# Kernel tuning notes

Hardware: AMD Instinct MI355X
Metric: run time of the kernel (lower is better)

Reference implementation:

```python
import jax, jax.numpy as jnp
import numpy as np

N_NODES = 100000
N_EDGES = 20000
NNZ = 800000
D_IN = 256
D_OUT = 256


def _segment_mean(feats, seg_ids, num_segments):
    # feats: [nnz, d] gathered features; seg_ids: [nnz] target segment per entry
    s = jax.ops.segment_sum(feats, seg_ids, num_segments=num_segments)
    cnt = jax.ops.segment_sum(jnp.ones((seg_ids.shape[0],), feats.dtype), seg_ids,
                              num_segments=num_segments)
    return s / jnp.maximum(cnt, 1.0)[:, None]


def setup_inputs() -> dict:
    key = jax.random.key(0)
    k1, k2, k3, k4, k5 = jax.random.split(key, 5)
    X = jax.random.normal(k1, (N_NODES, D_IN), dtype=jnp.float32)
    W = jax.random.normal(k2, (D_IN, D_OUT), dtype=jnp.float32) * (1.0 / np.sqrt(D_IN))
    b = jax.random.normal(k3, (D_OUT,), dtype=jnp.float32) * 0.01
    vertex_idx = jax.random.randint(k4, (NNZ,), 0, N_NODES, dtype=jnp.int32)
    edge_idx = jax.random.randint(k5, (NNZ,), 0, N_EDGES, dtype=jnp.int32)
    return {"X": X, "W": W, "b": b, "vertex_idx": vertex_idx, "edge_idx": edge_idx}


def reference(X, W, b, vertex_idx, edge_idx):
    # theta: linear projection
    H = X @ W + b                                   # [N_NODES, D_OUT]
    # v2e mean: hyperedge feature = mean of incident vertex features
    Y = _segment_mean(H[vertex_idx], edge_idx, N_EDGES)   # [N_EDGES, D_OUT]
    # e2v mean: vertex feature = mean of incident hyperedge features
    X_ = _segment_mean(Y[edge_idx], vertex_idx, N_NODES)  # [N_NODES, D_OUT]
    # ReLU; dropout is identity in eval mode
    return jax.nn.relu(X_)
```

## Files before the change

### kernel.cpp

```cpp
#include <hip/hip_runtime.h>
#include <hip/hip_bf16.h>

constexpr int N_NODES = 100000;
constexpr int N_EDGES = 20000;
constexpr int NNZ     = 800000;
constexpr int D       = 256;

typedef unsigned short ushort_t;
typedef unsigned short ushort4v __attribute__((ext_vector_type(4)));
typedef unsigned short ushort8v __attribute__((ext_vector_type(8)));
typedef __bf16         bf16x8   __attribute__((ext_vector_type(8)));
typedef float          f32x4    __attribute__((ext_vector_type(4)));
typedef float          f32x8    __attribute__((ext_vector_type(8)));

static __device__ inline ushort_t f2bf(float f) {
  unsigned u = __builtin_bit_cast(unsigned, f);
  return (ushort_t)((u + 0x7FFFu + ((u >> 16) & 1u)) >> 16);
}

static __device__ inline f32x8 row_f32(const ushort_t* p) {
  bf16x8 b = __builtin_bit_cast(bf16x8, *(const ushort8v*)p);
  return __builtin_convertvector(b, f32x8);
}

constexpr int HIST_BLOCKS  = 782;
constexpr int TRANS_BLOCKS = 64;
constexpr int CAST_BLOCKS  = 6250;
constexpr int PREP_BLOCKS  = HIST_BLOCKS + TRANS_BLOCKS + CAST_BLOCKS;

__global__ __launch_bounds__(256) void prep_kernel(
    const float* __restrict__ X, const float* __restrict__ W,
    const int* __restrict__ vidx, const int* __restrict__ eidx,
    ushort_t* __restrict__ Xb, ushort_t* __restrict__ Wt,
    int* __restrict__ ncnt, int* __restrict__ ecnt,
    int* __restrict__ erank, int* __restrict__ nrank) {
  const int blk = blockIdx.x, tid = threadIdx.x;
  if (blk < HIST_BLOCKS) {
    int i4 = blk * 256 + tid;
    if (i4 < NNZ / 4) {
      int4 e4 = ((const int4*)eidx)[i4];
      int4 v4 = ((const int4*)vidx)[i4];
      int4 er, nr;
      er.x = atomicAdd(&ecnt[e4.x], 1);  nr.x = atomicAdd(&ncnt[v4.x], 1);
      er.y = atomicAdd(&ecnt[e4.y], 1);  nr.y = atomicAdd(&ncnt[v4.y], 1);
      er.z = atomicAdd(&ecnt[e4.z], 1);  nr.z = atomicAdd(&ncnt[v4.z], 1);
      er.w = atomicAdd(&ecnt[e4.w], 1);  nr.w = atomicAdd(&ncnt[v4.w], 1);
      ((int4*)erank)[i4] = er;
      ((int4*)nrank)[i4] = nr;
    }
  } else if (blk < HIST_BLOCKS + TRANS_BLOCKS) {
    int wb = blk - HIST_BLOCKS;
#pragma unroll
    for (int i = 0; i < 4; ++i) {
      int k = wb * 4 + i;
      Wt[(size_t)tid * 256 + k] = f2bf(W[(size_t)k * 256 + tid]);
    }
  } else {
    int cb = blk - HIST_BLOCKS - TRANS_BLOCKS;
#pragma unroll
    for (int q = 0; q < 4; ++q) {
      int idx4 = cb * 1024 + q * 256 + tid;
      float4 v = ((const float4*)X)[idx4];
      ushort4v o = { f2bf(v.x), f2bf(v.y), f2bf(v.z), f2bf(v.w) };
      *(ushort4v*)&Xb[(size_t)idx4 * 4] = o;
    }
  }
}

constexpr int SCAN_L    = N_EDGES + N_NODES;
constexpr int SCAN_TPB  = 1024;
constexpr int SCAN_EPT  = 4;
constexpr int SCAN_TILE = SCAN_TPB * SCAN_EPT;
constexpr int SCAN_NB   = (SCAN_L + SCAN_TILE - 1) / SCAN_TILE;

__global__ __launch_bounds__(1024) void scan_phaseA(
    const int* __restrict__ cnt, int* __restrict__ comb, int* __restrict__ btot) {
  __shared__ int wsum[16];
  const int tid = threadIdx.x, lane = tid & 63, wid = tid >> 6;
  const int base = blockIdx.x * SCAN_TILE + tid * SCAN_EPT;
  int v[SCAN_EPT];
#pragma unroll
  for (int i = 0; i < SCAN_EPT; ++i) {
    int j = base + i;
    v[i] = (j < SCAN_L) ? cnt[j] : 0;
  }
  int tsum = v[0] + v[1] + v[2] + v[3];
  int x = tsum;
#pragma unroll
  for (int d = 1; d < 64; d <<= 1) {
    int y = __shfl_up(x, (unsigned)d, 64);
    if (lane >= d) x += y;
  }
  if (lane == 63) wsum[wid] = x;
  __syncthreads();
  if (wid == 0) {
    int s = (lane < 16) ? wsum[lane] : 0;
#pragma unroll
    for (int d = 1; d < 16; d <<= 1) {
      int y = __shfl_up(s, (unsigned)d, 64);
      if (lane >= d) s += y;
    }
    if (lane < 16) wsum[lane] = s;
  }
  __syncthreads();
  int texcl = ((wid == 0) ? 0 : wsum[wid - 1]) + (x - tsum);
  int run = texcl;
#pragma unroll
  for (int i = 0; i < SCAN_EPT; ++i) {
    int j = base + i;
    if (j < SCAN_L) comb[j] = run;
    run += v[i];
  }
  if (tid == 0) btot[blockIdx.x] = wsum[15];
}

__global__ void scan_phaseB(const int* __restrict__ btot, int* __restrict__ boff) {
  int lane = threadIdx.x;
  int v = (lane < SCAN_NB) ? btot[lane] : 0;
  int x = v;
#pragma unroll
  for (int d = 1; d < 64; d <<= 1) {
    int y = __shfl_up(x, (unsigned)d, 64);
    if (lane >= d) x += y;
  }
  if (lane < SCAN_NB) boff[lane] = x - v;
}

__global__ __launch_bounds__(1024) void scan_phaseC(
    const int* __restrict__ comb, const int* __restrict__ boff,
    int* __restrict__ eoff, int* __restrict__ noff) {
  const int base = blockIdx.x * SCAN_TILE + threadIdx.x * SCAN_EPT;
  const int add = boff[blockIdx.x];
#pragma unroll
  for (int i = 0; i < SCAN_EPT; ++i) {
    int j = base + i;
    if (j < SCAN_L) {
      int val = comb[j] + add;
      if (j < N_EDGES) eoff[j] = val;
      else             noff[j - N_EDGES] = val - NNZ;
    }
  }
  if (blockIdx.x == 0 && threadIdx.x == 0) {
    eoff[N_EDGES] = NNZ;
    noff[N_NODES] = NNZ;
  }
}

__global__ __launch_bounds__(256) void scatter_norank(
    const int* __restrict__ vidx, const int* __restrict__ eidx,
    const int* __restrict__ eoff, const int* __restrict__ noff,
    const int* __restrict__ erank, const int* __restrict__ nrank,
    int* __restrict__ evals, int* __restrict__ nvals) {
  int i4 = blockIdx.x * 256 + threadIdx.x;
  if (i4 < NNZ / 4) {
    int4 e4 = ((const int4*)eidx)[i4];
    int4 v4 = ((const int4*)vidx)[i4];
    int4 er = ((const int4*)erank)[i4];
    int4 nr = ((const int4*)nrank)[i4];
    evals[eoff[e4.x] + er.x] = v4.x;  nvals[noff[v4.x] + nr.x] = e4.x;
    evals[eoff[e4.y] + er.y] = v4.y;  nvals[noff[v4.y] + nr.y] = e4.y;
    evals[eoff[e4.z] + er.z] = v4.z;  nvals[noff[v4.z] + nr.z] = e4.z;
    evals[eoff[e4.w] + er.w] = v4.w;  nvals[noff[v4.w] + nr.w] = e4.w;
  }
}

__global__ __launch_bounds__(256) void v2e_mean(
    const ushort_t* __restrict__ Xb, const int* __restrict__ eoff,
    const int* __restrict__ evals, ushort_t* __restrict__ Xeb, int nseg) {
  int lane = threadIdx.x & 63;
  int half = lane >> 5, l32 = lane & 31;
  int seg  = blockIdx.x * 4 + (threadIdx.x >> 6);
  if (seg >= nseg) return;
  int s = eoff[seg], e = eoff[seg + 1];
  f32x8 acc = {0, 0, 0, 0, 0, 0, 0, 0};
  int j = s + half;
  for (; j + 6 < e; j += 8) {
    int r0 = evals[j], r1 = evals[j + 2], r2 = evals[j + 4], r3 = evals[j + 6];
    f32x8 f0 = row_f32(&Xb[(size_t)r0 * 256 + l32 * 8]);
    f32x8 f1 = row_f32(&Xb[(size_t)r1 * 256 + l32 * 8]);
    f32x8 f2 = row_f32(&Xb[(size_t)r2 * 256 + l32 * 8]);
    f32x8 f3 = row_f32(&Xb[(size_t)r3 * 256 + l32 * 8]);
    acc += (f0 + f1) + (f2 + f3);
  }
  for (; j < e; j += 2)
    acc += row_f32(&Xb[(size_t)evals[j] * 256 + l32 * 8]);
  float r[8];
#pragma unroll
  for (int i = 0; i < 8; ++i) r[i] = acc[i] + __shfl_down(acc[i], 32);
  if (half == 0) {
    float inv = 1.0f / (float)max(e - s, 1);
    ushort8v o;
#pragma unroll
    for (int i = 0; i < 8; ++i) o[i] = f2bf(r[i] * inv);
    *(ushort8v*)&Xeb[(size_t)seg * 256 + l32 * 8] = o;
  }
}

__global__ __launch_bounds__(256) void gemm_mfma(
    const ushort_t* __restrict__ A, const ushort_t* __restrict__ Wt,
    const float* __restrict__ bias, ushort_t* __restrict__ Ye) {
  const int w = threadIdx.x >> 6, lane = threadIdx.x & 63;
  const int m15 = lane & 15, q = lane >> 4;
  const int m0 = blockIdx.x * 16;
  const ushort_t* arow = A + (size_t)(m0 + m15) * 256 + q * 8;
  f32x4 acc[4] = { {0,0,0,0}, {0,0,0,0}, {0,0,0,0}, {0,0,0,0} };
  for (int k0 = 0; k0 < 256; k0 += 32) {
    bf16x8 af = __builtin_bit_cast(bf16x8, *(const ushort8v*)(arow + k0));
#pragma unroll
    for (int t = 0; t < 4; ++t) {
      const ushort_t* brow = Wt + (size_t)(w * 64 + t * 16 + m15) * 256 + k0 + q * 8;
      bf16x8 bf = __builtin_bit_cast(bf16x8, *(const ushort8v*)brow);
      acc[t] = __builtin_amdgcn_mfma_f32_16x16x32_bf16(af, bf, acc[t], 0, 0, 0);
    }
  }
#pragma unroll
  for (int t = 0; t < 4; ++t) {
    int col = w * 64 + t * 16 + m15;
    float bv = bias[col];
#pragma unroll
    for (int r = 0; r < 4; ++r) {
      int row = m0 + q * 4 + r;
      Ye[(size_t)row * 256 + col] = f2bf(acc[t][r] + bv);
    }
  }
}

__global__ __launch_bounds__(256) void e2v_mean_relu(
    const ushort_t* __restrict__ Yeb, const int* __restrict__ noff,
    const int* __restrict__ nvals, float* __restrict__ dst, int nseg) {
  int lane = threadIdx.x & 63;
  int half = lane >> 5, l32 = lane & 31;
  int seg  = blockIdx.x * 4 + (threadIdx.x >> 6);
  if (seg >= nseg) return;
  int s = noff[seg], e = noff[seg + 1];
  f32x8 acc = {0, 0, 0, 0, 0, 0, 0, 0};
  int j = s + half;
  for (; j + 6 < e; j += 8) {
    int r0 = nvals[j], r1 = nvals[j + 2], r2 = nvals[j + 4], r3 = nvals[j + 6];
    f32x8 f0 = row_f32(&Yeb[(size_t)r0 * 256 + l32 * 8]);
    f32x8 f1 = row_f32(&Yeb[(size_t)r1 * 256 + l32 * 8]);
    f32x8 f2 = row_f32(&Yeb[(size_t)r2 * 256 + l32 * 8]);
    f32x8 f3 = row_f32(&Yeb[(size_t)r3 * 256 + l32 * 8]);
    acc += (f0 + f1) + (f2 + f3);
  }
  for (; j < e; j += 2)
    acc += row_f32(&Yeb[(size_t)nvals[j] * 256 + l32 * 8]);
  float r[8];
#pragma unroll
  for (int i = 0; i < 8; ++i) r[i] = acc[i] + __shfl_down(acc[i], 32);
  if (half == 0) {
    float inv = 1.0f / (float)max(e - s, 1);
    float4 o0, o1;
    o0.x = fmaxf(r[0] * inv, 0.f); o0.y = fmaxf(r[1] * inv, 0.f);
    o0.z = fmaxf(r[2] * inv, 0.f); o0.w = fmaxf(r[3] * inv, 0.f);
    o1.x = fmaxf(r[4] * inv, 0.f); o1.y = fmaxf(r[5] * inv, 0.f);
    o1.z = fmaxf(r[6] * inv, 0.f); o1.w = fmaxf(r[7] * inv, 0.f);
    size_t base = (size_t)seg * 256 + l32 * 8;
    *(float4*)&dst[base]     = o0;
    *(float4*)&dst[base + 4] = o1;
  }
}

constexpr size_t OFF_XB    = 0;
constexpr size_t OFF_XEB   = OFF_XB  + (size_t)N_NODES * D * 2;
constexpr size_t OFF_YEB   = OFF_XEB + (size_t)N_EDGES * D * 2;
constexpr size_t OFF_WT    = OFF_YEB + (size_t)N_EDGES * D * 2;
constexpr size_t OFF_ZERO  = OFF_WT  + (size_t)D * D * 2;
constexpr size_t OFF_ECNT  = OFF_ZERO;
constexpr size_t OFF_NCNT  = OFF_ECNT + (size_t)N_EDGES * 4;
constexpr size_t ZERO_BYTES = (size_t)(N_EDGES + N_NODES) * 4;
constexpr size_t OFF_EOFF  = OFF_ZERO + ZERO_BYTES;
constexpr size_t OFF_NOFF  = OFF_EOFF + (size_t)(N_EDGES + 1 + 3) * 4;
constexpr size_t OFF_EVALS = OFF_NOFF + (size_t)(N_NODES + 1 + 3) * 4;
constexpr size_t OFF_NVALS = OFF_EVALS + (size_t)NNZ * 4;
constexpr size_t OFF_ERANK = OFF_NVALS + (size_t)NNZ * 4;
constexpr size_t OFF_NRANK = OFF_ERANK + (size_t)NNZ * 4;
constexpr size_t OFF_COMB  = OFF_NRANK + (size_t)NNZ * 4;
constexpr size_t OFF_BTOT  = OFF_COMB + (size_t)SCAN_L * 4;
constexpr size_t OFF_BOFF  = OFF_BTOT + 128;

extern "C" void kernel_launch(void* const* d_in, const int* in_sizes, int n_in,
                              void* d_out, int out_size, void* d_ws, size_t ws_size,
                              hipStream_t stream) {
  const float* X    = (const float*)d_in[0];
  const float* W    = (const float*)d_in[1];
  const float* b    = (const float*)d_in[2];
  const int*   vidx = (const int*)d_in[3];
  const int*   eidx = (const int*)d_in[4];
  float*       out  = (float*)d_out;

  char* ws = (char*)d_ws;
  ushort_t* Xb   = (ushort_t*)(ws + OFF_XB);
  ushort_t* Xeb  = (ushort_t*)(ws + OFF_XEB);
  ushort_t* Yeb  = (ushort_t*)(ws + OFF_YEB);
  ushort_t* Wt   = (ushort_t*)(ws + OFF_WT);
  int* ecnt  = (int*)(ws + OFF_ECNT);
  int* ncnt  = (int*)(ws + OFF_NCNT);
  int* eoff  = (int*)(ws + OFF_EOFF);
  int* noff  = (int*)(ws + OFF_NOFF);
  int* evals = (int*)(ws + OFF_EVALS);
  int* nvals = (int*)(ws + OFF_NVALS);
  int* erank = (int*)(ws + OFF_ERANK);
  int* nrank = (int*)(ws + OFF_NRANK);
  int* comb  = (int*)(ws + OFF_COMB);
  int* btot  = (int*)(ws + OFF_BTOT);
  int* boff  = (int*)(ws + OFF_BOFF);

  hipMemsetAsync(ws + OFF_ZERO, 0, ZERO_BYTES, stream);

  prep_kernel<<<PREP_BLOCKS, 256, 0, stream>>>(X, W, vidx, eidx, Xb, Wt,
                                               ncnt, ecnt, erank, nrank);

  scan_phaseA<<<SCAN_NB, SCAN_TPB, 0, stream>>>(ecnt, comb, btot);
  scan_phaseB<<<1, 64, 0, stream>>>(btot, boff);
  scan_phaseC<<<SCAN_NB, SCAN_TPB, 0, stream>>>(comb, boff, eoff, noff);

  scatter_norank<<<(NNZ / 4 + 255) / 256, 256, 0, stream>>>(
      vidx, eidx, eoff, noff, erank, nrank, evals, nvals);

  v2e_mean<<<(N_EDGES + 3) / 4, 256, 0, stream>>>(Xb, eoff, evals, Xeb, N_EDGES);

  gemm_mfma<<<N_EDGES / 16, 256, 0, stream>>>(Xeb, Wt, b, Yeb);

  e2v_mean_relu<<<(N_NODES + 3) / 4, 256, 0, stream>>>(Yeb, noff, nvals, out, N_NODES);
}
```

Before: 422.2 us.

## Replace global atomic histogram with LDS byte-packed per-chunk histograms

Measured after the change: 423.9 us. About the same (+0.4%).

```diff
diff --git a/kernel.cpp b/kernel.cpp
--- a/kernel.cpp
+++ b/kernel.cpp
@@ -23,30 +23,60 @@
   return __builtin_convertvector(b, f32x8);
 }
 
-constexpr int HIST_BLOCKS  = 782;
+static __device__ inline int bsum(unsigned long long x) {
+  return (int)((x * 0x0101010101010101ULL) >> 56);
+}
+
+constexpr int HCHUNKS   = 8;
+constexpr int CHUNK     = NNZ / HCHUNKS;
+constexpr int CHUNK4    = CHUNK / 4;
+constexpr int NH_RANGES = 5;
+constexpr int NH_BINS   = N_NODES / NH_RANGES;
+constexpr int NH_BLOCKS = NH_RANGES * HCHUNKS;
+constexpr int EH_BLOCKS = HCHUNKS;
+constexpr int HIST_BLOCKS  = NH_BLOCKS + EH_BLOCKS;
 constexpr int TRANS_BLOCKS = 64;
 constexpr int CAST_BLOCKS  = 6250;
 constexpr int PREP_BLOCKS  = HIST_BLOCKS + TRANS_BLOCKS + CAST_BLOCKS;
+constexpr int HWORDS = 5000;
 
 __global__ __launch_bounds__(256) void prep_kernel(
     const float* __restrict__ X, const float* __restrict__ W,
     const int* __restrict__ vidx, const int* __restrict__ eidx,
     ushort_t* __restrict__ Xb, ushort_t* __restrict__ Wt,
-    int* __restrict__ ncnt, int* __restrict__ ecnt,
-    int* __restrict__ erank, int* __restrict__ nrank) {
+    unsigned char* __restrict__ pe, unsigned char* __restrict__ pn,
+    unsigned char* __restrict__ lre, unsigned char* __restrict__ lrn) {
+  __shared__ unsigned int hist[HWORDS];
   const int blk = blockIdx.x, tid = threadIdx.x;
   if (blk < HIST_BLOCKS) {
-    int i4 = blk * 256 + tid;
-    if (i4 < NNZ / 4) {
-      int4 e4 = ((const int4*)eidx)[i4];
-      int4 v4 = ((const int4*)vidx)[i4];
-      int4 er, nr;
-      er.x = atomicAdd(&ecnt[e4.x], 1);  nr.x = atomicAdd(&ncnt[v4.x], 1);
-      er.y = atomicAdd(&ecnt[e4.y], 1);  nr.y = atomicAdd(&ncnt[v4.y], 1);
-      er.z = atomicAdd(&ecnt[e4.z], 1);  nr.z = atomicAdd(&ncnt[v4.z], 1);
-      er.w = atomicAdd(&ecnt[e4.w], 1);  nr.w = atomicAdd(&ncnt[v4.w], 1);
-      ((int4*)erank)[i4] = er;
-      ((int4*)nrank)[i4] = nr;
+    const bool is_n = blk < NH_BLOCKS;
+    const int c  = is_n ? (blk & 7) : (blk - NH_BLOCKS);
+    const int lo = is_n ? (blk >> 3) * NH_BINS : 0;
+    const int* __restrict__ idx = is_n ? vidx : eidx;
+    unsigned char* __restrict__ lr = is_n ? lrn : lre;
+    for (int t = tid; t < HWORDS; t += 256) hist[t] = 0;
+    __syncthreads();
+    const int base4 = c * CHUNK4;
+#pragma unroll 2
+    for (int k = tid; k < CHUNK4; k += 256) {
+      int i4 = base4 + k;
+      int4 q = ((const int4*)idx)[i4];
+      int vv[4] = {q.x, q.y, q.z, q.w};
+#pragma unroll
+      for (int j = 0; j < 4; ++j) {
+        unsigned rel = (unsigned)(vv[j] - lo);
+        if (rel < (unsigned)NH_BINS) {
+          unsigned sh = 8u * (rel & 3u);
+          unsigned old = atomicAdd(&hist[rel >> 2], 1u << sh);
+          lr[(size_t)i4 * 4 + j] = (unsigned char)((old >> sh) & 0xFFu);
+        }
+      }
+    }
+    __syncthreads();
+    unsigned char* __restrict__ pb = is_n ? pn : pe;
+    for (int t = tid; t < NH_BINS; t += 256) {
+      unsigned byte = (hist[t >> 2] >> (8u * (t & 3u))) & 0xFFu;
+      pb[(size_t)(lo + t) * 8 + c] = (unsigned char)byte;
     }
   } else if (blk < HIST_BLOCKS + TRANS_BLOCKS) {
     int wb = blk - HIST_BLOCKS;
@@ -74,7 +104,9 @@
 constexpr int SCAN_NB   = (SCAN_L + SCAN_TILE - 1) / SCAN_TILE;
 
 __global__ __launch_bounds__(1024) void scan_phaseA(
-    const int* __restrict__ cnt, int* __restrict__ comb, int* __restrict__ btot) {
+    const unsigned long long* __restrict__ pe,
+    const unsigned long long* __restrict__ pn,
+    int* __restrict__ comb, int* __restrict__ btot) {
   __shared__ int wsum[16];
   const int tid = threadIdx.x, lane = tid & 63, wid = tid >> 6;
   const int base = blockIdx.x * SCAN_TILE + tid * SCAN_EPT;
@@ -82,7 +114,9 @@
 #pragma unroll
   for (int i = 0; i < SCAN_EPT; ++i) {
     int j = base + i;
-    v[i] = (j < SCAN_L) ? cnt[j] : 0;
+    int x = 0;
+    if (j < SCAN_L) x = bsum(j < N_EDGES ? pe[j] : pn[j - N_EDGES]);
+    v[i] = x;
   }
   int tsum = v[0] + v[1] + v[2] + v[3];
   int x = tsum;
@@ -114,23 +148,12 @@
   if (tid == 0) btot[blockIdx.x] = wsum[15];
 }
 
-__global__ void scan_phaseB(const int* __restrict__ btot, int* __restrict__ boff) {
-  int lane = threadIdx.x;
-  int v = (lane < SCAN_NB) ? btot[lane] : 0;
-  int x = v;
-#pragma unroll
-  for (int d = 1; d < 64; d <<= 1) {
-    int y = __shfl_up(x, (unsigned)d, 64);
-    if (lane >= d) x += y;
-  }
-  if (lane < SCAN_NB) boff[lane] = x - v;
-}
-
 __global__ __launch_bounds__(1024) void scan_phaseC(
-    const int* __restrict__ comb, const int* __restrict__ boff,
+    const int* __restrict__ comb, const int* __restrict__ btot,
     int* __restrict__ eoff, int* __restrict__ noff) {
+  int add = 0;
+  for (int bdx = 0; bdx < blockIdx.x; ++bdx) add += btot[bdx];
   const int base = blockIdx.x * SCAN_TILE + threadIdx.x * SCAN_EPT;
-  const int add = boff[blockIdx.x];
 #pragma unroll
   for (int i = 0; i < SCAN_EPT; ++i) {
     int j = base + i;
@@ -146,21 +169,30 @@
   }
 }
 
-__global__ __launch_bounds__(256) void scatter_norank(
+__global__ __launch_bounds__(256) void scatter_calc(
     const int* __restrict__ vidx, const int* __restrict__ eidx,
     const int* __restrict__ eoff, const int* __restrict__ noff,
-    const int* __restrict__ erank, const int* __restrict__ nrank,
+    const unsigned long long* __restrict__ pe,
+    const unsigned long long* __restrict__ pn,
+    const unsigned char* __restrict__ lre, const unsigned char* __restrict__ lrn,
     int* __restrict__ evals, int* __restrict__ nvals) {
   int i4 = blockIdx.x * 256 + threadIdx.x;
-  if (i4 < NNZ / 4) {
-    int4 e4 = ((const int4*)eidx)[i4];
-    int4 v4 = ((const int4*)vidx)[i4];
-    int4 er = ((const int4*)erank)[i4];
-    int4 nr = ((const int4*)nrank)[i4];
-    evals[eoff[e4.x] + er.x] = v4.x;  nvals[noff[v4.x] + nr.x] = e4.x;
-    evals[eoff[e4.y] + er.y] = v4.y;  nvals[noff[v4.y] + nr.y] = e4.y;
-    evals[eoff[e4.z] + er.z] = v4.z;  nvals[noff[v4.z] + nr.z] = e4.z;
-    evals[eoff[e4.w] + er.w] = v4.w;  nvals[noff[v4.w] + nr.w] = e4.w;
+  if (i4 >= NNZ / 4) return;
+  int c = i4 / CHUNK4;
+  unsigned long long mask = (1ULL << (8 * c)) - 1ULL;
+  int4 e4 = ((const int4*)eidx)[i4];
+  int4 v4 = ((const int4*)vidx)[i4];
+  unsigned le = *(const unsigned*)(lre + (size_t)i4 * 4);
+  unsigned ln = *(const unsigned*)(lrn + (size_t)i4 * 4);
+  int ee[4] = {e4.x, e4.y, e4.z, e4.w};
+  int vv[4] = {v4.x, v4.y, v4.z, v4.w};
+#pragma unroll
+  for (int j = 0; j < 4; ++j) {
+    int e = ee[j], v = vv[j];
+    int re = (int)((le >> (8 * j)) & 0xFFu);
+    int rn = (int)((ln >> (8 * j)) & 0xFFu);
+    evals[eoff[e] + bsum(pe[e] & mask) + re] = v;
+    nvals[noff[v] + bsum(pn[v] & mask) + rn] = e;
   }
 }
 
@@ -265,19 +297,16 @@
 constexpr size_t OFF_XEB   = OFF_XB  + (size_t)N_NODES * D * 2;
 constexpr size_t OFF_YEB   = OFF_XEB + (size_t)N_EDGES * D * 2;
 constexpr size_t OFF_WT    = OFF_YEB + (size_t)N_EDGES * D * 2;
-constexpr size_t OFF_ZERO  = OFF_WT  + (size_t)D * D * 2;
-constexpr size_t OFF_ECNT  = OFF_ZERO;
-constexpr size_t OFF_NCNT  = OFF_ECNT + (size_t)N_EDGES * 4;
-constexpr size_t ZERO_BYTES = (size_t)(N_EDGES + N_NODES) * 4;
-constexpr size_t OFF_EOFF  = OFF_ZERO + ZERO_BYTES;
+constexpr size_t OFF_PE    = OFF_WT  + (size_t)D * D * 2;
+constexpr size_t OFF_PN    = OFF_PE  + (size_t)N_EDGES * 8;
+constexpr size_t OFF_LRE   = OFF_PN  + (size_t)N_NODES * 8;
+constexpr size_t OFF_LRN   = OFF_LRE + (size_t)NNZ;
+constexpr size_t OFF_EOFF  = OFF_LRN + (size_t)NNZ;
 constexpr size_t OFF_NOFF  = OFF_EOFF + (size_t)(N_EDGES + 1 + 3) * 4;
 constexpr size_t OFF_EVALS = OFF_NOFF + (size_t)(N_NODES + 1 + 3) * 4;
 constexpr size_t OFF_NVALS = OFF_EVALS + (size_t)NNZ * 4;
-constexpr size_t OFF_ERANK = OFF_NVALS + (size_t)NNZ * 4;
-constexpr size_t OFF_NRANK = OFF_ERANK + (size_t)NNZ * 4;
-constexpr size_t OFF_COMB  = OFF_NRANK + (size_t)NNZ * 4;
+constexpr size_t OFF_COMB  = OFF_NVALS + (size_t)NNZ * 4;
 constexpr size_t OFF_BTOT  = OFF_COMB + (size_t)SCAN_L * 4;
-constexpr size_t OFF_BOFF  = OFF_BTOT + 128;
 
 extern "C" void kernel_launch(void* const* d_in, const int* in_sizes, int n_in,
                               void* d_out, int out_size, void* d_ws, size_t ws_size,
@@ -294,29 +323,28 @@
   ushort_t* Xeb  = (ushort_t*)(ws + OFF_XEB);
   ushort_t* Yeb  = (ushort_t*)(ws + OFF_YEB);
   ushort_t* Wt   = (ushort_t*)(ws + OFF_WT);
-  int* ecnt  = (int*)(ws + OFF_ECNT);
-  int* ncnt  = (int*)(ws + OFF_NCNT);
+  unsigned char* pe_b = (unsigned char*)(ws + OFF_PE);
+  unsigned char* pn_b = (unsigned char*)(ws + OFF_PN);
+  unsigned long long* pe_u = (unsigned long long*)(ws + OFF_PE);
+  unsigned long long* pn_u = (unsigned long long*)(ws + OFF_PN);
+  unsigned char* lre = (unsigned char*)(ws + OFF_LRE);
+  unsigned char* lrn = (unsigned char*)(ws + OFF_LRN);
   int* eoff  = (int*)(ws + OFF_EOFF);
   int* noff  = (int*)(ws + OFF_NOFF);
   int* evals = (int*)(ws + OFF_EVALS);
   int* nvals = (int*)(ws + OFF_NVALS);
-  int* erank = (int*)(ws + OFF_ERANK);
-  int* nrank = (int*)(ws + OFF_NRANK);
   int* comb  = (int*)(ws + OFF_COMB);
   int* btot  = (int*)(ws + OFF_BTOT);
-  int* boff  = (int*)(ws + OFF_BOFF);
-
-  hipMemsetAsync(ws + OFF_ZERO, 0, ZERO_BYTES, stream);
+
 
   prep_kernel<<<PREP_BLOCKS, 256, 0, stream>>>(X, W, vidx, eidx, Xb, Wt,
-                                               ncnt, ecnt, erank, nrank);
-
-  scan_phaseA<<<SCAN_NB, SCAN_TPB, 0, stream>>>(ecnt, comb, btot);
-  scan_phaseB<<<1, 64, 0, stream>>>(btot, boff);
-  scan_phaseC<<<SCAN_NB, SCAN_TPB, 0, stream>>>(comb, boff, eoff, noff);
-
-  scatter_norank<<<(NNZ / 4 + 255) / 256, 256, 0, stream>>>(
-      vidx, eidx, eoff, noff, erank, nrank, evals, nvals);
+                                               pe_b, pn_b, lre, lrn);
+
+  scan_phaseA<<<SCAN_NB, SCAN_TPB, 0, stream>>>(pe_u, pn_u, comb, btot);
+  scan_phaseC<<<SCAN_NB, SCAN_TPB, 0, stream>>>(comb, btot, eoff, noff);
+
+  scatter_calc<<<(NNZ / 4 + 255) / 256, 256, 0, stream>>>(
+      vidx, eidx, eoff, noff, pe_u, pn_u, lre, lrn, evals, nvals);
 
   v2e_mean<<<(N_EDGES + 3) / 4, 256, 0, stream>>>(Xb, eoff, evals, Xeb, N_EDGES);
 
```
